# Kernel optimization log

Measured on AMD Instinct MI355X. Metric: run time of the kernel, lower is better.

## Reference

```python
import jax, jax.numpy as jnp
import numpy as np

PI = np.pi
EPS_A = 1e-4


def _frft_1d(x, a):
    """Chirp-z shear FRFT along the last axis. x: complex (..., N), a: scalar order."""
    a = jnp.clip(a, EPS_A, 2.0 - EPS_A)
    N = x.shape[-1]
    x = jnp.fft.ifftshift(x, axes=-1)
    alpha = a * PI / 2.0
    tan_a2 = jnp.tan(a * PI / 4.0)
    sin_a = jnp.sin(alpha)
    n = (jnp.arange(N, dtype=jnp.float32) - (N // 2))  # [-N/2, N/2)
    c1 = jnp.exp(-1j * PI * (n ** 2) * tan_a2 / N)      # chirp (depends on a)
    c2 = jnp.exp(-1j * PI * (n ** 2) / (N * sin_a))     # kernel chirp
    y = jnp.fft.ifft(jnp.fft.fft(x * c1, axis=-1) * c2, axis=-1)
    y = y * c1 / jnp.sqrt(jnp.abs(sin_a) + 1e-12)
    return jnp.fft.fftshift(y, axes=-1)


def _frft2d(x, ax, ay):
    # width pass (last axis) with ay, then height pass with ax -- same math as the
    # per-row / per-column torch loops, fully batched.
    y = _frft_1d(x, ay)                                   # over W
    y = jnp.swapaxes(_frft_1d(jnp.swapaxes(y, -1, -2), ax), -1, -2)  # over H
    return y


def setup_inputs() -> dict:
    key = jax.random.key(0)
    kx, = jax.random.split(key, 1)
    B, C, H, W = 4, 32, 256, 256
    x = jax.random.normal(kx, (B, C, H, W), dtype=jnp.float32)
    alpha = jnp.float32(0.5)
    # 1x1 conv weight (C, 2C): module init = copy of magnitude channels
    w = jnp.zeros((C, 2 * C), dtype=jnp.float32)
    w = w.at[jnp.arange(C), jnp.arange(C)].set(1.0)
    return {"x": x, "alpha": alpha, "w": w}


def reference(x, alpha, w):
    Xc = x.astype(jnp.complex64)
    Y = _frft2d(Xc, alpha, alpha)                        # (B, C, H, W) complex
    out = jnp.concatenate([jnp.abs(Y), jnp.angle(Y) / PI], axis=1)  # (B, 2C, H, W)
    out = jnp.einsum('oc,bchw->bohw', w, out)            # 1x1 conv, no bias
    return out.astype(x.dtype)
```

## Files before the change

kernel.cpp:

```cpp
#include <hip/hip_runtime.h>
#include <math.h>

#define B_N 4
#define C_N 32
#define H_N 256
#define W_N 256
#define PI_D 3.14159265358979323846
#define LSQ 257
#define LDW 260

typedef _Float16 half8 __attribute__((ext_vector_type(8)));
typedef float f32x4 __attribute__((ext_vector_type(4)));

__device__ __forceinline__ float2 cmul(float2 a, float2 b) {
    return make_float2(a.x * b.x - a.y * b.y, a.x * b.y + a.y * b.x);
}
__device__ __forceinline__ float2 f2add(float2 a, float2 b) {
    return make_float2(a.x + b.x, a.y + b.y);
}
__device__ __forceinline__ float2 f2sub(float2 a, float2 b) {
    return make_float2(a.x - b.x, a.y - b.y);
}

__device__ __forceinline__ void make_tables(int tid, const float* __restrict__ alpha_p,
                                            float2* c1l, float2* c2l, float2* twl,
                                            float* sscl) {
    if (tid < 256) {
        int j = tid;
        double a = fmin(fmax((double)alpha_p[0], 1e-4), 2.0 - 1e-4);
        double tan_a2 = tan(a * PI_D / 4.0);
        double sin_a  = sin(a * PI_D / 2.0);
        double n = (double)(j - 128);
        float sn, cs;

        double u1 = n * n * tan_a2 * (1.0 / 256.0);
        u1 -= 2.0 * floor(u1 * 0.5);
        __sincosf((float)(-PI_D * u1), &sn, &cs);
        c1l[j] = make_float2(cs, sn);

        double u2 = n * n / (256.0 * sin_a);
        u2 -= 2.0 * floor(u2 * 0.5);
        __sincosf((float)(-PI_D * u2), &sn, &cs);
        c2l[j] = make_float2(cs, sn);

        int k1 = j >> 4, t = j & 15;
        __sincosf((float)(-2.0 * PI_D * (double)(t * k1) * (1.0 / 256.0)), &sn, &cs);
        twl[j] = make_float2(cs, sn);

        if (j == 0) *sscl = (float)(1.0 / sqrt(fabs(sin_a) + 1e-12));
    }
}

template <bool INV>
__device__ __forceinline__ void fft16(float2* v) {
    const float C1 = 0.9238795325112867f, S1 = 0.3826834323650898f;
    const float C2 = 0.7071067811865476f;
    const float2 tw1 = make_float2(C1, INV ? S1 : -S1);
    const float2 tw2 = make_float2(C2, INV ? C2 : -C2);
    const float2 tw3 = make_float2(S1, INV ? C1 : -C1);
    const float2 tw4 = make_float2(0.0f, INV ? 1.0f : -1.0f);
    const float2 tw6 = make_float2(-C2, INV ? C2 : -C2);
    const float2 tw9 = make_float2(-C1, INV ? -S1 : S1);
    float2 u[16];
    #pragma unroll
    for (int n2 = 0; n2 < 4; ++n2) {
        float2 e0 = v[n2], e1 = v[4 + n2], e2 = v[8 + n2], e3 = v[12 + n2];
        float2 t0 = f2add(e0, e2), t1 = f2sub(e0, e2);
        float2 t2 = f2add(e1, e3), t3 = f2sub(e1, e3);
        float2 A0 = f2add(t0, t2);
        float2 A2 = f2sub(t0, t2);
        float2 A1, A3;
        if (!INV) { A1 = make_float2(t1.x + t3.y, t1.y - t3.x);
                    A3 = make_float2(t1.x - t3.y, t1.y + t3.x); }
        else      { A1 = make_float2(t1.x - t3.y, t1.y + t3.x);
                    A3 = make_float2(t1.x + t3.y, t1.y - t3.x); }
        u[n2] = A0;
        if (n2 == 0) { u[4 + n2] = A1;            u[8 + n2] = A2;            u[12 + n2] = A3; }
        if (n2 == 1) { u[4 + n2] = cmul(A1, tw1); u[8 + n2] = cmul(A2, tw2); u[12 + n2] = cmul(A3, tw3); }
        if (n2 == 2) { u[4 + n2] = cmul(A1, tw2); u[8 + n2] = cmul(A2, tw4); u[12 + n2] = cmul(A3, tw6); }
        if (n2 == 3) { u[4 + n2] = cmul(A1, tw3); u[8 + n2] = cmul(A2, tw6); u[12 + n2] = cmul(A3, tw9); }
    }
    #pragma unroll
    for (int k1 = 0; k1 < 4; ++k1) {
        float2 e0 = u[4 * k1], e1 = u[4 * k1 + 1], e2 = u[4 * k1 + 2], e3 = u[4 * k1 + 3];
        float2 t0 = f2add(e0, e2), t1 = f2sub(e0, e2);
        float2 t2 = f2add(e1, e3), t3 = f2sub(e1, e3);
        v[4 * k1 + 0] = f2add(t0, t2);
        v[4 * k1 + 2] = f2sub(t0, t2);
        if (!INV) { v[4 * k1 + 1] = make_float2(t1.x + t3.y, t1.y - t3.x);
                    v[4 * k1 + 3] = make_float2(t1.x - t3.y, t1.y + t3.x); }
        else      { v[4 * k1 + 1] = make_float2(t1.x - t3.y, t1.y + t3.x);
                    v[4 * k1 + 3] = make_float2(t1.x + t3.y, t1.y - t3.x); }
    }
}
#define REG(k) (4 * ((k) & 3) + ((k) >> 2))

__device__ __forceinline__ void frft_core16(float2* v, float2* __restrict__ sp,
                                            int t,
                                            const float2* __restrict__ c2l,
                                            const float2* __restrict__ twl) {
    fft16<false>(v);
    float2 w[16];
    #pragma unroll
    for (int k1 = 0; k1 < 16; ++k1)
        w[k1] = cmul(v[REG(k1)], twl[16 * k1 + t]);
    #pragma unroll
    for (int k1 = 0; k1 < 16; ++k1)
        sp[16 * k1 + (t ^ k1)] = w[k1];
    __syncthreads();
    #pragma unroll
    for (int n2 = 0; n2 < 16; ++n2)
        v[n2] = sp[16 * t + (n2 ^ t)];
    fft16<false>(v);
    #pragma unroll
    for (int k2 = 0; k2 < 16; ++k2)
        w[k2] = cmul(v[REG(k2)], c2l[t + 16 * k2]);
    fft16<true>(w);
    __syncthreads();
    #pragma unroll
    for (int m2 = 0; m2 < 16; ++m2) {
        float2 tw = twl[16 * m2 + t];
        tw.y = -tw.y;
        sp[16 * m2 + (t ^ m2)] = cmul(w[REG(m2)], tw);
    }
    __syncthreads();
    #pragma unroll
    for (int k1 = 0; k1 < 16; ++k1)
        v[k1] = sp[16 * t + (k1 ^ t)];
    fft16<true>(v);
}

__global__ __launch_bounds__(512, 4) void frft_cols_real(
        const float* __restrict__ x,
        const float* __restrict__ alpha_p,
        float2* __restrict__ Y) {
    __shared__ float2 s[32 * LSQ];
    __shared__ float2 c1l[256], c2l[256], twl[256];
    __shared__ float sscl;
    int tid = threadIdx.x;

    int blk = blockIdx.x;
    int w0 = (blk & 7) << 5;
    long long bc = blk >> 3;
    const float* xb = x + (bc << 16) + w0;

    float4 xv[4];
    #pragma unroll
    for (int p = 0; p < 4; ++p) {
        int idx = tid + (p << 9);
        int row = idx >> 3, c4 = idx & 7;
        xv[p] = *(const float4*)(xb + row * W_N + (c4 << 2));
    }

    make_tables(tid, alpha_p, c1l, c2l, twl, &sscl);

    float* fs = (float*)s;
    #pragma unroll
    for (int p = 0; p < 4; ++p) {
        int idx = tid + (p << 9);
        int row = idx >> 3, c4 = idx & 7;
        fs[(4 * c4 + 0) * (2 * LSQ) + row] = xv[p].x;
        fs[(4 * c4 + 1) * (2 * LSQ) + row] = xv[p].y;
        fs[(4 * c4 + 2) * (2 * LSQ) + row] = xv[p].z;
        fs[(4 * c4 + 3) * (2 * LSQ) + row] = xv[p].w;
    }
    __syncthreads();

    int seq = tid & 31, t = tid >> 5;
    float xs[16];
    #pragma unroll
    for (int n1 = 0; n1 < 16; ++n1)
        xs[n1] = fs[seq * (2 * LSQ) + 16 * (n1 ^ 8) + t];
    float scl_v = sscl;
    __syncthreads();

    float2 v[16];
    #pragma unroll
    for (int n1 = 0; n1 < 16; ++n1) {
        float2 c = c1l[16 * n1 + t];
        v[n1] = make_float2(xs[n1] * c.x, xs[n1] * c.y);
    }

    frft_core16(v, s + seq * LSQ, t, c2l, twl);

    float sc = scl_v * (1.0f / 256.0f);
    float2* Yb = Y + (bc << 16) + w0 + seq;
    #pragma unroll
    for (int m1 = 0; m1 < 16; ++m1) {
        float2 o = cmul(v[REG(m1)], c1l[16 * m1 + t]);
        Yb[(16 * (m1 ^ 8) + t) * W_N] = make_float2(o.x * sc, o.y * sc);
    }
}

__device__ __forceinline__ float fast_atan2(float y, float x) {
    float ax = fabsf(x), ay = fabsf(y);
    float mx = fmaxf(ax, ay), mn = fminf(ax, ay);
    float z = mn * __builtin_amdgcn_rcpf(fmaxf(mx, 1e-37f));
    float z2 = z * z;
    float p = fmaf(z2, -0.01172120f, 0.05265332f);
    p = fmaf(z2, p, -0.11643287f);
    p = fmaf(z2, p, 0.19354346f);
    p = fmaf(z2, p, -0.33262347f);
    p = fmaf(z2, p, 0.99997726f);
    p = p * z;
    float r = (ay > ax) ? (1.5707963f - p) : p;
    r = (x < 0.0f) ? (3.14159265f - r) : r;
    return copysignf(r, y);
}

__global__ __launch_bounds__(512, 4) void frft_rows_conv(
        const float2* __restrict__ Y,
        const float* __restrict__ alpha_p,
        const float* __restrict__ wmat, float* __restrict__ out) {
    __shared__ float2 s[32 * LSQ];
    __shared__ float2 c1l[256], c2l[256], twl[256];
    __shared__ float sscl;
    int tid = threadIdx.x;
    int t = tid & 15, ch = tid >> 4;

    int b = blockIdx.x >> 8, h = blockIdx.x & 255;
    const float2* xr = Y + (((long long)(b * C_N + ch)) << 16) + (h << 8);

    float2 v[16];
    #pragma unroll
    for (int n1 = 0; n1 < 16; ++n1)
        v[n1] = xr[16 * (n1 ^ 8) + t];

    make_tables(tid, alpha_p, c1l, c2l, twl, &sscl);
    __syncthreads();

    #pragma unroll
    for (int n1 = 0; n1 < 16; ++n1)
        v[n1] = cmul(v[n1], c1l[16 * n1 + t]);

    float2* sp = s + ch * LSQ;
    frft_core16(v, sp, t, c2l, twl);

    float sc = sscl * (1.0f / 256.0f);
    #pragma unroll
    for (int m1 = 0; m1 < 16; ++m1) {
        float2 o = cmul(v[REG(m1)], c1l[16 * m1 + t]);
        float mg = sc * sqrtf(fmaf(o.x, o.x, o.y * o.y));
        float an = fast_atan2(o.y, o.x) * 0.31830988618f;
        sp[16 * (m1 ^ 8) + t] = make_float2(mg, an);
    }
    __syncthreads();

    int lane = tid & 63, wv = tid >> 6;
    int q = lane >> 4, l15 = lane & 15;

    half8 bf[2][2];
    #pragma unroll
    for (int nt = 0; nt < 2; ++nt)
        #pragma unroll
        for (int kt = 0; kt < 2; ++kt) {
            const float* wp = wmat + (nt * 16 + l15) * 64 + kt * 32 + q * 8;
            float4 wa = *(const float4*)wp;
            float4 wb = *(const float4*)(wp + 4);
            bf[nt][kt][0] = (_Float16)wa.x; bf[nt][kt][1] = (_Float16)wa.y;
            bf[nt][kt][2] = (_Float16)wa.z; bf[nt][kt][3] = (_Float16)wa.w;
            bf[nt][kt][4] = (_Float16)wb.x; bf[nt][kt][5] = (_Float16)wb.y;
            bf[nt][kt][6] = (_Float16)wb.z; bf[nt][kt][7] = (_Float16)wb.w;
        }

    f32x4 acc[2][2];
    #pragma unroll
    for (int i = 0; i < 2; ++i)
        #pragma unroll
        for (int j = 0; j < 2; ++j)
            acc[i][j] = (f32x4){0.0f, 0.0f, 0.0f, 0.0f};

    #pragma unroll
    for (int mt2 = 0; mt2 < 2; ++mt2) {
        int mt = wv * 2 + mt2;
        int w = mt * 16 + l15;
        half8 am, aa;
        #pragma unroll
        for (int j = 0; j < 8; ++j) {
            float2 fv = s[(q * 8 + j) * LSQ + w];
            am[j] = (_Float16)fv.x;
            aa[j] = (_Float16)fv.y;
        }
        #pragma unroll
        for (int nt = 0; nt < 2; ++nt) {
            acc[mt2][nt] = __builtin_amdgcn_mfma_f32_16x16x32_f16(am, bf[nt][0], acc[mt2][nt], 0, 0, 0);
            acc[mt2][nt] = __builtin_amdgcn_mfma_f32_16x16x32_f16(aa, bf[nt][1], acc[mt2][nt], 0, 0, 0);
        }
    }
    __syncthreads();

    float* Ob = (float*)s;
    #pragma unroll
    for (int mt2 = 0; mt2 < 2; ++mt2) {
        int mt = wv * 2 + mt2;
        #pragma unroll
        for (int nt = 0; nt < 2; ++nt) {
            int o = nt * 16 + l15;
            *(f32x4*)&Ob[o * LDW + mt * 16 + q * 4] = acc[mt2][nt];
        }
    }
    __syncthreads();

    int o2 = tid >> 4, i16 = tid & 15;
    float* ob = out + (((long long)(b * C_N + o2)) << 16) + (h << 8);
    #pragma unroll
    for (int p = 0; p < 4; ++p) {
        int w4 = i16 * 4 + (p << 6);
        f32x4 val = *(f32x4*)&Ob[o2 * LDW + w4];
        *(f32x4*)(ob + w4) = val;
    }
}

extern "C" void kernel_launch(void* const* d_in, const int* in_sizes, int n_in,
                              void* d_out, int out_size, void* d_ws, size_t ws_size,
                              hipStream_t stream) {
    const float* x     = (const float*)d_in[0];
    const float* alpha = (const float*)d_in[1];
    const float* wmat  = (const float*)d_in[2];
    float* out = (float*)d_out;

    float2* Y = (float2*)d_ws;

    frft_cols_real<<<B_N * C_N * (W_N / 32), 512, 0, stream>>>(x, alpha, Y);

    frft_rows_conv<<<B_N * H_N, 512, 0, stream>>>(Y, alpha, wmat, out);
}
```

Before: 130.9 us.

## Use wave barriers in row FRFT core, float tables, vectorized transpose staging

In the row pass, each 16-thread FFT group sits inside one 64-wide wavefront, so the three block-wide __syncthreads in the FFT core are replaced by wave barriers. This removes cross-wave stalls there. The chirp and twiddle tables are now computed in float instead of double, which avoids slow FP64 tan/sin/floor. The column pass stages input as row-major float4 stores with a padded stride of 36 instead of scalar transposed stores. The risks are reduced table precision for large n² phases and a reliance on wave-synchronous LDS ordering being correct.

```diff
diff --git a/kernel.cpp b/kernel.cpp
--- a/kernel.cpp
+++ b/kernel.cpp
@@ -8,6 +8,7 @@
 #define PI_D 3.14159265358979323846
 #define LSQ 257
 #define LDW 260
+#define LTS 36
 
 typedef _Float16 half8 __attribute__((ext_vector_type(8)));
 typedef float f32x4 __attribute__((ext_vector_type(4)));
@@ -27,27 +28,28 @@
                                             float* sscl) {
     if (tid < 256) {
         int j = tid;
-        double a = fmin(fmax((double)alpha_p[0], 1e-4), 2.0 - 1e-4);
-        double tan_a2 = tan(a * PI_D / 4.0);
-        double sin_a  = sin(a * PI_D / 2.0);
-        double n = (double)(j - 128);
+        float a = fminf(fmaxf(alpha_p[0], 1e-4f), 2.0f - 1e-4f);
+        float tan_a2 = tanf(a * (float)(PI_D / 4.0));
+        float sin_a  = sinf(a * (float)(PI_D / 2.0));
+        float n = (float)(j - 128);
+        float n2f = n * n;
         float sn, cs;
 
-        double u1 = n * n * tan_a2 * (1.0 / 256.0);
-        u1 -= 2.0 * floor(u1 * 0.5);
-        __sincosf((float)(-PI_D * u1), &sn, &cs);
+        float u1 = n2f * tan_a2 * (1.0f / 256.0f);
+        u1 -= 2.0f * floorf(u1 * 0.5f);
+        __sincosf(-(float)PI_D * u1, &sn, &cs);
         c1l[j] = make_float2(cs, sn);
 
-        double u2 = n * n / (256.0 * sin_a);
-        u2 -= 2.0 * floor(u2 * 0.5);
-        __sincosf((float)(-PI_D * u2), &sn, &cs);
+        float u2 = n2f / (256.0f * sin_a);
+        u2 -= 2.0f * floorf(u2 * 0.5f);
+        __sincosf(-(float)PI_D * u2, &sn, &cs);
         c2l[j] = make_float2(cs, sn);
 
         int k1 = j >> 4, t = j & 15;
-        __sincosf((float)(-2.0 * PI_D * (double)(t * k1) * (1.0 / 256.0)), &sn, &cs);
+        __sincosf(-(float)(2.0 * PI_D / 256.0) * (float)(t * k1), &sn, &cs);
         twl[j] = make_float2(cs, sn);
 
-        if (j == 0) *sscl = (float)(1.0 / sqrt(fabs(sin_a) + 1e-12));
+        if (j == 0) *sscl = 1.0f / sqrtf(sin_a + 1e-12f);
     }
 }
 
@@ -95,6 +97,13 @@
 }
 #define REG(k) (4 * ((k) & 3) + ((k) >> 2))
 
+template <bool WL>
+__device__ __forceinline__ void core_sync() {
+    if (WL) __builtin_amdgcn_wave_barrier();
+    else    __syncthreads();
+}
+
+template <bool WL>
 __device__ __forceinline__ void frft_core16(float2* v, float2* __restrict__ sp,
                                             int t,
                                             const float2* __restrict__ c2l,
@@ -107,7 +116,7 @@
     #pragma unroll
     for (int k1 = 0; k1 < 16; ++k1)
         sp[16 * k1 + (t ^ k1)] = w[k1];
-    __syncthreads();
+    core_sync<WL>();
     #pragma unroll
     for (int n2 = 0; n2 < 16; ++n2)
         v[n2] = sp[16 * t + (n2 ^ t)];
@@ -116,14 +125,14 @@
     for (int k2 = 0; k2 < 16; ++k2)
         w[k2] = cmul(v[REG(k2)], c2l[t + 16 * k2]);
     fft16<true>(w);
-    __syncthreads();
+    core_sync<WL>();
     #pragma unroll
     for (int m2 = 0; m2 < 16; ++m2) {
         float2 tw = twl[16 * m2 + t];
         tw.y = -tw.y;
         sp[16 * m2 + (t ^ m2)] = cmul(w[REG(m2)], tw);
     }
-    __syncthreads();
+    core_sync<WL>();
     #pragma unroll
     for (int k1 = 0; k1 < 16; ++k1)
         v[k1] = sp[16 * t + (k1 ^ t)];
@@ -159,10 +168,7 @@
     for (int p = 0; p < 4; ++p) {
         int idx = tid + (p << 9);
         int row = idx >> 3, c4 = idx & 7;
-        fs[(4 * c4 + 0) * (2 * LSQ) + row] = xv[p].x;
-        fs[(4 * c4 + 1) * (2 * LSQ) + row] = xv[p].y;
-        fs[(4 * c4 + 2) * (2 * LSQ) + row] = xv[p].z;
-        fs[(4 * c4 + 3) * (2 * LSQ) + row] = xv[p].w;
+        *(float4*)&fs[row * LTS + (c4 << 2)] = xv[p];
     }
     __syncthreads();
 
@@ -170,7 +176,7 @@
     float xs[16];
     #pragma unroll
     for (int n1 = 0; n1 < 16; ++n1)
-        xs[n1] = fs[seq * (2 * LSQ) + 16 * (n1 ^ 8) + t];
+        xs[n1] = fs[(16 * (n1 ^ 8) + t) * LTS + seq];
     float scl_v = sscl;
     __syncthreads();
 
@@ -181,7 +187,7 @@
         v[n1] = make_float2(xs[n1] * c.x, xs[n1] * c.y);
     }
 
-    frft_core16(v, s + seq * LSQ, t, c2l, twl);
+    frft_core16<false>(v, s + seq * LSQ, t, c2l, twl);
 
     float sc = scl_v * (1.0f / 256.0f);
     float2* Yb = Y + (bc << 16) + w0 + seq;
@@ -234,7 +240,7 @@
         v[n1] = cmul(v[n1], c1l[16 * n1 + t]);
 
     float2* sp = s + ch * LSQ;
-    frft_core16(v, sp, t, c2l, twl);
+    frft_core16<true>(v, sp, t, c2l, twl);
 
     float sc = sscl * (1.0f / 256.0f);
     #pragma unroll
```

Result: no change. 132.3 us (+1.1%).
